# Optimization experiments

Hardware: AMD Instinct MI355X
Metric: run time of the kernel (lower is better)

The kernel has to match this reference:

```python
import jax, jax.numpy as jnp
import numpy as np

B, T, VOCAB = 65536, 34, 14
D_MODEL, TOK_DIM, POS_DIM, QK_DIM, FFN = 5, 2, 3, 5, 2
MAX_DIGITS = 10
EPS = 1e-5


def setup_inputs() -> dict:
    key = jax.random.key(0)
    ks = jax.random.split(key, 8)
    return dict(
        idx=jax.random.randint(ks[0], (B, T), 0, VOCAB),
        tok_A=jnp.float32(2.5), tok_start=jnp.float32(-1.2), tok_stride=jnp.float32(0.29),
        sp_amp=jnp.float32(3.5), sp_phase=jnp.float32(0.0), sp_slope=jnp.float32(0.15), sp_offset=jnp.float32(0.0),
        norm_w=jnp.ones((D_MODEL,), jnp.float32),
        q_w=jax.random.normal(ks[1], (QK_DIM, POS_DIM), jnp.float32) * 0.5,
        q_phase=jnp.zeros((1,), jnp.float32),
        out_A=jax.random.normal(ks[2], (D_MODEL, 1), jnp.float32) * 0.45,
        out_B=jax.random.normal(ks[3], (1, D_MODEL), jnp.float32) * 0.2,
        fc1_w=jax.random.normal(ks[4], (FFN, D_MODEL), jnp.float32) * 0.4,
        fc2_w=jax.random.normal(ks[5], (D_MODEL, FFN), jnp.float32) * 0.4,
        head_w=jax.random.normal(ks[6], (TOK_DIM, D_MODEL), jnp.float32) * 0.4,
    )


def rmsnorm(x, w):
    rms = jnp.sqrt(jnp.mean(x * x, axis=-1, keepdims=True) + EPS)
    return x / rms * w


def micro_forward(idx, tok_A, tok_start, tok_stride, sp_amp, sp_phase, sp_slope, sp_offset,
                  norm_w, q_w, q_phase, out_A, out_B, fc1_w, fc2_w, head_w):
    # token arc embedding table (V, 2)
    d = jnp.arange(VOCAB, dtype=jnp.float32)
    ang = tok_start + d * tok_stride
    tok_emb = jnp.stack([tok_A * jnp.cos(ang), tok_A * jnp.sin(ang)], axis=-1)
    # spiral positional embedding (T, 3)
    t = jnp.arange(T, dtype=jnp.float32)
    th = 2.0 * jnp.pi * t / MAX_DIGITS + sp_phase
    pos = jnp.stack([sp_amp * jnp.cos(th), sp_amp * jnp.sin(th), sp_slope * t + sp_offset], axis=-1)
    # embed: concat token (B,T,2) + position (T,3) -> (B,T,5)
    x = jnp.concatenate([tok_emb[idx], jnp.broadcast_to(pos, (idx.shape[0], T, POS_DIM))], axis=-1)
    # attention (pre-norm); q/k from positions only (qk_input='pos'), shared across batch
    h = rmsnorm(x, norm_w)
    k = pos @ q_w.T                       # (T, QK)
    c, s = jnp.cos(q_phase[0]), jnp.sin(q_phase[0])
    q = k.at[:, 0].set(c * k[:, 0] - s * k[:, 1]).at[:, 1].set(s * k[:, 0] + c * k[:, 1])
    scores = (q @ k.T) / jnp.sqrt(jnp.float32(QK_DIM))   # (T, T)
    causal = jnp.tril(jnp.ones((T, T), bool))
    attn = jax.nn.softmax(jnp.where(causal, scores, -1e9), axis=-1)
    attn_out = jnp.einsum('ts,bsd->btd', attn, h)         # v = normed x (head_dim = d_model)
    x = x + (attn_out @ out_A) @ out_B                    # rank-1 out_proj, residual
    # FFN (pre-norm, 2 hidden units)
    h2 = rmsnorm(x, norm_w)
    x = x + jax.nn.relu(h2 @ fc1_w.T) @ fc2_w.T
    # head: project to token plane, read out against arc embedding table
    hf = rmsnorm(x, norm_w)
    logits = (hf @ head_w.T) @ tok_emb.T                  # (B, T, V)
    return logits


def reference(idx, tok_A, tok_start, tok_stride, sp_amp, sp_phase, sp_slope, sp_offset,
              norm_w, q_w, q_phase, out_A, out_B, fc1_w, fc2_w, head_w):
    return micro_forward(idx, tok_A, tok_start, tok_stride, sp_amp, sp_phase, sp_slope, sp_offset,
                         norm_w, q_w, q_phase, out_A, out_B, fc1_w, fc2_w, head_w)
```

## Files before the change

kernel.cpp:

```cpp
#include <hip/hip_runtime.h>
#include <math.h>

#define T 34
#define V 14
#define NT 256
#define NBLK 2176
#define NWAVES 8704
#define LIM (65536 * 34)

typedef float f32x4 __attribute__((ext_vector_type(4)));


__global__ void setup_k(const float* __restrict__ tokA_p, const float* __restrict__ tokStart_p,
                        const float* __restrict__ tokStride_p, const float* __restrict__ spAmp_p,
                        const float* __restrict__ spPhase_p, const float* __restrict__ spSlope_p,
                        const float* __restrict__ spOffset_p, const float* __restrict__ norm_w,
                        const float* __restrict__ q_w, const float* __restrict__ q_phase,
                        const float* __restrict__ out_A, float* __restrict__ ws)
{
    __shared__ float sPOS[T][3];
    __shared__ float sK[T][5];
    __shared__ float sQ[T][5];
    __shared__ float sTE[V][2];
    __shared__ float sA[T][35];

    const int tid = threadIdx.x;

    if (tid < V) {
        float ang = tokStart_p[0] + (float)tid * tokStride_p[0];
        float c = tokA_p[0] * cosf(ang), s = tokA_p[0] * sinf(ang);
        sTE[tid][0] = c; sTE[tid][1] = s;
        ws[1680 + 2 * tid] = c; ws[1681 + 2 * tid] = s;
    }
    if (tid < T) {
        float th = (float)tid * 0.62831853071795864769f + spPhase_p[0];
        float p0 = spAmp_p[0] * cosf(th), p1 = spAmp_p[0] * sinf(th);
        float p2 = spSlope_p[0] * (float)tid + spOffset_p[0];
        sPOS[tid][0] = p0; sPOS[tid][1] = p1; sPOS[tid][2] = p2;
        ws[1708 + 3 * tid] = p0; ws[1709 + 3 * tid] = p1; ws[1710 + 3 * tid] = p2;
        float kk[5];
        #pragma unroll
        for (int i = 0; i < 5; ++i)
            kk[i] = p0 * q_w[3 * i] + p1 * q_w[3 * i + 1] + p2 * q_w[3 * i + 2];
        float cc = cosf(q_phase[0]), ss = sinf(q_phase[0]);
        #pragma unroll
        for (int i = 0; i < 5; ++i) sK[tid][i] = kk[i];
        sQ[tid][0] = cc * kk[0] - ss * kk[1];
        sQ[tid][1] = ss * kk[0] + cc * kk[1];
        sQ[tid][2] = kk[2]; sQ[tid][3] = kk[3]; sQ[tid][4] = kk[4];
    }
    __syncthreads();

    if (tid < T) {
        const int t = tid;
        float mx = -1e30f;
        for (int s = 0; s <= t; ++s) {
            float d = (sQ[t][0] * sK[s][0] + sQ[t][1] * sK[s][1] + sQ[t][2] * sK[s][2]
                     + sQ[t][3] * sK[s][3] + sQ[t][4] * sK[s][4]) * 0.44721359549995793928f;
            sA[t][s] = d;
            mx = fmaxf(mx, d);
        }
        float sum = 0.f;
        for (int s = 0; s <= t; ++s) { float e = expf(sA[t][s] - mx); sA[t][s] = e; sum += e; }
        float inv = 1.f / sum;
        for (int s = 0; s < 35; ++s) ws[t * 35 + s] = (s <= t) ? sA[t][s] * inv : 0.f;
    }
    for (int e = tid; e < 490; e += 64) {
        int v = e / 35, s = e - v * 35;
        float g = 0.f;
        if (s < T) {
            float x0 = sTE[v][0], x1 = sTE[v][1];
            float x2 = sPOS[s][0], x3 = sPOS[s][1], x4 = sPOS[s][2];
            float ms = (x0*x0 + x1*x1 + x2*x2 + x3*x3 + x4*x4) * 0.2f;
            float r = rsqrtf(ms + 1e-5f);
            g = (x0 * norm_w[0] * out_A[0] + x1 * norm_w[1] * out_A[1]
               + x2 * norm_w[2] * out_A[2] + x3 * norm_w[3] * out_A[3]
               + x4 * norm_w[4] * out_A[4]) * r;
        }
        ws[1190 + e] = g;
    }
}

__global__ __launch_bounds__(NT, 4) void micro_main(
    const int* __restrict__ idx, const float* __restrict__ ws, float* __restrict__ out,
    const float* __restrict__ norm_w, const float* __restrict__ out_B,
    const float* __restrict__ fc1_w, const float* __restrict__ fc2_w,
    const float* __restrict__ head_w)
{
    __shared__ float G_lds[V * 35];
    __shared__ float TE_lds[V * 2];
    __shared__ float gbW[4][2][104];
    __shared__ float stageAll[4 * 896];

    const int tid = threadIdx.x;
    const int w = tid >> 6, lane = tid & 63;
    const int wid = blockIdx.x * 4 + w;

    for (int i = tid; i < 490; i += NT) G_lds[i] = ws[1190 + i];
    if (tid < 28) TE_lds[tid] = ws[1680 + tid];
    __syncthreads();

    const int t = (wid * 64 + lane) % T;
    float A[T];
    #pragma unroll
    for (int s = 0; s < T; ++s) A[s] = ws[t * 35 + s];
    const float ps0 = ws[1708 + 3 * t], ps1 = ws[1709 + 3 * t], ps2 = ws[1710 + 3 * t];

    const float nw0 = norm_w[0], nw1 = norm_w[1], nw2 = norm_w[2], nw3 = norm_w[3], nw4 = norm_w[4];
    const float oB0 = out_B[0], oB1 = out_B[1], oB2 = out_B[2], oB3 = out_B[3], oB4 = out_B[4];
    float w1[2][5], hw[2][5], w20[5], w21[5];
    #pragma unroll
    for (int j = 0; j < 2; ++j)
        #pragma unroll
        for (int d = 0; d < 5; ++d) { w1[j][d] = fc1_w[j*5+d]; hw[j][d] = head_w[j*5+d]; }
    #pragma unroll
    for (int d = 0; d < 5; ++d) { w20[d] = fc2_w[2*d]; w21[d] = fc2_w[2*d+1]; }
    float te0[V], te1[V];
    #pragma unroll
    for (int v = 0; v < V; ++v) { te0[v] = ws[1680 + 2*v]; te1[v] = ws[1681 + 2*v]; }

    const int s_a = (lane < T) ? lane : lane - T;
    const int i2 = lane + 64;
    const int s_b = (i2 < 68) ? i2 - 34 : i2 - 68;
    const bool act2 = (i2 < 102);

    float* gbA = gbW[w][0];
    float* gbB = gbW[w][1];
    float* stg = stageAll + w * 896;
    float2* stg2 = reinterpret_cast<float2*>(stg);
    const f32x4* st4 = reinterpret_cast<const f32x4*>(stg);

    auto computeItem = [&](int tile, int rbase, int curtok, const float* gbT) {
        float acc0 = 0.f, acc1 = 0.f;
        const float2* gbp = reinterpret_cast<const float2*>(gbT + rbase);
        #pragma unroll
        for (int s = 0; s < 17; ++s) {
            float2 gg = gbp[s];
            acc0 = fmaf(A[2*s],   gg.x, acc0);
            acc1 = fmaf(A[2*s+1], gg.y, acc1);
        }
        float acc = acc0 + acc1;

        float2 te = *reinterpret_cast<const float2*>(&TE_lds[curtok * 2]);
        float x0 = te.x + acc * oB0;
        float x1 = te.y + acc * oB1;
        float x2 = ps0 + acc * oB2;
        float x3 = ps1 + acc * oB3;
        float x4 = ps2 + acc * oB4;

        float ms = (x0*x0 + x1*x1 + x2*x2 + x3*x3 + x4*x4) * 0.2f;
        float rr = rsqrtf(ms + 1e-5f);
        float h0 = x0*rr*nw0, h1 = x1*rr*nw1, h2 = x2*rr*nw2, h3 = x3*rr*nw3, h4 = x4*rr*nw4;
        float f0 = fmaxf(0.f, h0*w1[0][0] + h1*w1[0][1] + h2*w1[0][2] + h3*w1[0][3] + h4*w1[0][4]);
        float f1 = fmaxf(0.f, h0*w1[1][0] + h1*w1[1][1] + h2*w1[1][2] + h3*w1[1][3] + h4*w1[1][4]);
        x0 += f0*w20[0] + f1*w21[0];
        x1 += f0*w20[1] + f1*w21[1];
        x2 += f0*w20[2] + f1*w21[2];
        x3 += f0*w20[3] + f1*w21[3];
        x4 += f0*w20[4] + f1*w21[4];

        ms = (x0*x0 + x1*x1 + x2*x2 + x3*x3 + x4*x4) * 0.2f;
        rr = rsqrtf(ms + 1e-5f);
        h0 = x0*rr*nw0; h1 = x1*rr*nw1; h2 = x2*rr*nw2; h3 = x3*rr*nw3; h4 = x4*rr*nw4;
        float p0 = h0*hw[0][0] + h1*hw[0][1] + h2*hw[0][2] + h3*hw[0][3] + h4*hw[0][4];
        float p1 = h0*hw[1][0] + h1*hw[1][1] + h2*hw[1][2] + h3*hw[1][3] + h4*hw[1][4];

        #pragma unroll
        for (int j = 0; j < 7; ++j) {
            float2 o2;
            o2.x = p0 * te0[2*j]   + p1 * te1[2*j];
            o2.y = p0 * te0[2*j+1] + p1 * te1[2*j+1];
            stg2[lane * 7 + j] = o2;
        }
        f32x4* outp = reinterpret_cast<f32x4*>(out) + (size_t)tile * 224;
        __builtin_nontemporal_store(st4[lane],       outp + lane);
        __builtin_nontemporal_store(st4[lane + 64],  outp + lane + 64);
        __builtin_nontemporal_store(st4[lane + 128], outp + lane + 128);
        if (lane < 32)
            __builtin_nontemporal_store(st4[lane + 192], outp + lane + 192);
    };

    int tileA = wid, tileB = wid + NWAVES;
    int b0A = (tileA * 64) / T, b0B = (tileB * 64) / T;
    int tk0A = idx[b0A * T + lane];
    int tk1A = idx[min(b0A * T + lane + 64, LIM - 1)];
    int tkoA = idx[tileA * 64 + lane];
    int tk0B = idx[b0B * T + lane];
    int tk1B = idx[min(b0B * T + lane + 64, LIM - 1)];
    int tkoB = idx[tileB * 64 + lane];

    #pragma unroll
    for (int it = 0; it < 2; ++it) {
        gbA[lane] = G_lds[tk0A * 35 + s_a];
        if (act2) gbA[i2] = G_lds[tk1A * 35 + s_b];
        gbB[lane] = G_lds[tk0B * 35 + s_a];
        if (act2) gbB[i2] = G_lds[tk1B * 35 + s_b];

        const int rbA = ((tileA * 64 + lane) / T - b0A) * T;
        const int rbB = ((tileB * 64 + lane) / T - b0B) * T;
        const int ctA = tkoA, ctB = tkoB;
        const int tA = tileA, tB = tileB;

        if (it == 0) {
            tileA += 2 * NWAVES; tileB += 2 * NWAVES;
            b0A = (tileA * 64) / T; b0B = (tileB * 64) / T;
            tk0A = idx[b0A * T + lane];
            tk1A = idx[min(b0A * T + lane + 64, LIM - 1)];
            tkoA = idx[tileA * 64 + lane];
            tk0B = idx[b0B * T + lane];
            tk1B = idx[min(b0B * T + lane + 64, LIM - 1)];
            tkoB = idx[tileB * 64 + lane];
        }

        computeItem(tA, rbA, ctA, gbA);
        computeItem(tB, rbB, ctB, gbB);
    }
}

extern "C" void kernel_launch(void* const* d_in, const int* in_sizes, int n_in,
                              void* d_out, int out_size, void* d_ws, size_t ws_size,
                              hipStream_t stream) {
    const int*   idx        = (const int*)  d_in[0];
    const float* tok_A      = (const float*)d_in[1];
    const float* tok_start  = (const float*)d_in[2];
    const float* tok_stride = (const float*)d_in[3];
    const float* sp_amp     = (const float*)d_in[4];
    const float* sp_phase   = (const float*)d_in[5];
    const float* sp_slope   = (const float*)d_in[6];
    const float* sp_offset  = (const float*)d_in[7];
    const float* norm_w     = (const float*)d_in[8];
    const float* q_w        = (const float*)d_in[9];
    const float* q_phase    = (const float*)d_in[10];
    const float* out_A      = (const float*)d_in[11];
    const float* out_B      = (const float*)d_in[12];
    const float* fc1_w      = (const float*)d_in[13];
    const float* fc2_w      = (const float*)d_in[14];
    const float* head_w     = (const float*)d_in[15];
    float* out = (float*)d_out;
    float* ws  = (float*)d_ws;

    setup_k<<<1, 64, 0, stream>>>(tok_A, tok_start, tok_stride, sp_amp, sp_phase,
                                  sp_slope, sp_offset, norm_w, q_w, q_phase, out_A, ws);
    micro_main<<<NBLK, NT, 0, stream>>>(idx, ws, out, norm_w, out_B, fc1_w, fc2_w, head_w);
}
```

Baseline: 39.57 us.

## Fuse setup kernel into main kernel, recomputing shared tables per block

Removes the separate single-block setup launch and its workspace round trip. Each block of the main kernel now computes the token and position embeddings, the causal softmax attention matrix and the G table in LDS, and reuses the staging buffer as scratch for this. This drops one launch and the serial dependency on a tiny one-block kernel. In exchange every block repeats the setup arithmetic (trig, exp and the 34x34 scores) and adds extra barriers before the main work.

```diff
diff --git a/kernel.cpp b/kernel.cpp
--- a/kernel.cpp
+++ b/kernel.cpp
@@ -10,101 +10,111 @@
 
 typedef float f32x4 __attribute__((ext_vector_type(4)));
 
-
-__global__ void setup_k(const float* __restrict__ tokA_p, const float* __restrict__ tokStart_p,
-                        const float* __restrict__ tokStride_p, const float* __restrict__ spAmp_p,
-                        const float* __restrict__ spPhase_p, const float* __restrict__ spSlope_p,
-                        const float* __restrict__ spOffset_p, const float* __restrict__ norm_w,
-                        const float* __restrict__ q_w, const float* __restrict__ q_phase,
-                        const float* __restrict__ out_A, float* __restrict__ ws)
+__global__ __launch_bounds__(NT, 4) void micro_fused(
+    const int* __restrict__ idx, float* __restrict__ out,
+    const float* __restrict__ p_tokA, const float* __restrict__ p_tokStart,
+    const float* __restrict__ p_tokStride, const float* __restrict__ p_spAmp,
+    const float* __restrict__ p_spPhase, const float* __restrict__ p_spSlope,
+    const float* __restrict__ p_spOffset, const float* __restrict__ norm_w,
+    const float* __restrict__ q_w, const float* __restrict__ q_phase,
+    const float* __restrict__ out_A, const float* __restrict__ out_B,
+    const float* __restrict__ fc1_w, const float* __restrict__ fc2_w,
+    const float* __restrict__ head_w)
 {
-    __shared__ float sPOS[T][3];
-    __shared__ float sK[T][5];
-    __shared__ float sQ[T][5];
-    __shared__ float sTE[V][2];
-    __shared__ float sA[T][35];
+    __shared__ float G_lds[V * 35];
+    __shared__ float TE_lds[V * 2];
+    __shared__ float POS_lds[T * 3];
+    __shared__ float gbW[4][2][104];
+    __shared__ float stageAll[4 * 896];
 
     const int tid = threadIdx.x;
+    const int w = tid >> 6, lane = tid & 63;
+    const int wid = blockIdx.x * 4 + w;
+
+    float* sA = stageAll;
+    float* sK = stageAll + 1200;
+    float* sQ = stageAll + 1370;
 
     if (tid < V) {
-        float ang = tokStart_p[0] + (float)tid * tokStride_p[0];
-        float c = tokA_p[0] * cosf(ang), s = tokA_p[0] * sinf(ang);
-        sTE[tid][0] = c; sTE[tid][1] = s;
-        ws[1680 + 2 * tid] = c; ws[1681 + 2 * tid] = s;
+        float ang = p_tokStart[0] + (float)tid * p_tokStride[0];
+        TE_lds[2 * tid]     = p_tokA[0] * cosf(ang);
+        TE_lds[2 * tid + 1] = p_tokA[0] * sinf(ang);
     }
     if (tid < T) {
-        float th = (float)tid * 0.62831853071795864769f + spPhase_p[0];
-        float p0 = spAmp_p[0] * cosf(th), p1 = spAmp_p[0] * sinf(th);
-        float p2 = spSlope_p[0] * (float)tid + spOffset_p[0];
-        sPOS[tid][0] = p0; sPOS[tid][1] = p1; sPOS[tid][2] = p2;
-        ws[1708 + 3 * tid] = p0; ws[1709 + 3 * tid] = p1; ws[1710 + 3 * tid] = p2;
+        float th = (float)tid * 0.62831853071795864769f + p_spPhase[0];
+        float p0 = p_spAmp[0] * cosf(th), p1 = p_spAmp[0] * sinf(th);
+        float p2 = p_spSlope[0] * (float)tid + p_spOffset[0];
+        POS_lds[3 * tid] = p0; POS_lds[3 * tid + 1] = p1; POS_lds[3 * tid + 2] = p2;
         float kk[5];
         #pragma unroll
         for (int i = 0; i < 5; ++i)
             kk[i] = p0 * q_w[3 * i] + p1 * q_w[3 * i + 1] + p2 * q_w[3 * i + 2];
         float cc = cosf(q_phase[0]), ss = sinf(q_phase[0]);
         #pragma unroll
-        for (int i = 0; i < 5; ++i) sK[tid][i] = kk[i];
-        sQ[tid][0] = cc * kk[0] - ss * kk[1];
-        sQ[tid][1] = ss * kk[0] + cc * kk[1];
-        sQ[tid][2] = kk[2]; sQ[tid][3] = kk[3]; sQ[tid][4] = kk[4];
-    }
-    __syncthreads();
-
-    if (tid < T) {
-        const int t = tid;
-        float mx = -1e30f;
-        for (int s = 0; s <= t; ++s) {
-            float d = (sQ[t][0] * sK[s][0] + sQ[t][1] * sK[s][1] + sQ[t][2] * sK[s][2]
-                     + sQ[t][3] * sK[s][3] + sQ[t][4] * sK[s][4]) * 0.44721359549995793928f;
-            sA[t][s] = d;
-            mx = fmaxf(mx, d);
-        }
-        float sum = 0.f;
-        for (int s = 0; s <= t; ++s) { float e = expf(sA[t][s] - mx); sA[t][s] = e; sum += e; }
-        float inv = 1.f / sum;
-        for (int s = 0; s < 35; ++s) ws[t * 35 + s] = (s <= t) ? sA[t][s] * inv : 0.f;
-    }
-    for (int e = tid; e < 490; e += 64) {
+        for (int i = 0; i < 5; ++i) sK[tid * 5 + i] = kk[i];
+        sQ[tid * 5 + 0] = cc * kk[0] - ss * kk[1];
+        sQ[tid * 5 + 1] = ss * kk[0] + cc * kk[1];
+        sQ[tid * 5 + 2] = kk[2]; sQ[tid * 5 + 3] = kk[3]; sQ[tid * 5 + 4] = kk[4];
+    }
+    __syncthreads();
+
+    for (int e = tid; e < T * T; e += NT) {
+        unsigned tt = (unsigned)e / (unsigned)T;
+        unsigned s  = (unsigned)e - tt * T;
+        if (s <= tt) {
+            float d = 0.f;
+            #pragma unroll
+            for (int i = 0; i < 5; ++i) d += sQ[tt * 5 + i] * sK[s * 5 + i];
+            sA[tt * 35 + s] = d * 0.44721359549995793928f;
+        }
+    }
+    for (int e = tid; e < V * 35; e += NT) {
         int v = e / 35, s = e - v * 35;
         float g = 0.f;
         if (s < T) {
-            float x0 = sTE[v][0], x1 = sTE[v][1];
-            float x2 = sPOS[s][0], x3 = sPOS[s][1], x4 = sPOS[s][2];
+            float x0 = TE_lds[2*v], x1 = TE_lds[2*v+1];
+            float x2 = POS_lds[3*s], x3 = POS_lds[3*s+1], x4 = POS_lds[3*s+2];
             float ms = (x0*x0 + x1*x1 + x2*x2 + x3*x3 + x4*x4) * 0.2f;
             float r = rsqrtf(ms + 1e-5f);
             g = (x0 * norm_w[0] * out_A[0] + x1 * norm_w[1] * out_A[1]
                + x2 * norm_w[2] * out_A[2] + x3 * norm_w[3] * out_A[3]
                + x4 * norm_w[4] * out_A[4]) * r;
         }
-        ws[1190 + e] = g;
-    }
-}
-
-__global__ __launch_bounds__(NT, 4) void micro_main(
-    const int* __restrict__ idx, const float* __restrict__ ws, float* __restrict__ out,
-    const float* __restrict__ norm_w, const float* __restrict__ out_B,
-    const float* __restrict__ fc1_w, const float* __restrict__ fc2_w,
-    const float* __restrict__ head_w)
-{
-    __shared__ float G_lds[V * 35];
-    __shared__ float TE_lds[V * 2];
-    __shared__ float gbW[4][2][104];
-    __shared__ float stageAll[4 * 896];
-
-    const int tid = threadIdx.x;
-    const int w = tid >> 6, lane = tid & 63;
-    const int wid = blockIdx.x * 4 + w;
-
-    for (int i = tid; i < 490; i += NT) G_lds[i] = ws[1190 + i];
-    if (tid < 28) TE_lds[tid] = ws[1680 + tid];
+        G_lds[e] = g;
+    }
+    __syncthreads();
+
+    if (tid < T) {
+        const int tt = tid;
+        float vals[T];
+        #pragma unroll
+        for (int s = 0; s < T; ++s) vals[s] = sA[tt * 35 + s];
+        float mx = -1e30f;
+        #pragma unroll
+        for (int s = 0; s < T; ++s) if (s <= tt) mx = fmaxf(mx, vals[s]);
+        float sum = 0.f;
+        #pragma unroll
+        for (int s = 0; s < T; ++s) {
+            float e2 = (s <= tt) ? expf(vals[s] - mx) : 0.f;
+            vals[s] = e2;
+            sum += e2;
+        }
+        float inv = 1.f / sum;
+        #pragma unroll
+        for (int s = 0; s < T; ++s) sA[tt * 35 + s] = vals[s] * inv;
+        sA[tt * 35 + 34] = 0.f;
+    }
     __syncthreads();
 
     const int t = (wid * 64 + lane) % T;
     float A[T];
     #pragma unroll
-    for (int s = 0; s < T; ++s) A[s] = ws[t * 35 + s];
-    const float ps0 = ws[1708 + 3 * t], ps1 = ws[1709 + 3 * t], ps2 = ws[1710 + 3 * t];
+    for (int s = 0; s < T; ++s) A[s] = sA[t * 35 + s];
+    const float ps0 = POS_lds[3*t], ps1 = POS_lds[3*t+1], ps2 = POS_lds[3*t+2];
+    float te0[V], te1[V];
+    #pragma unroll
+    for (int v = 0; v < V; ++v) { te0[v] = TE_lds[2*v]; te1[v] = TE_lds[2*v+1]; }
+    __syncthreads();
 
     const float nw0 = norm_w[0], nw1 = norm_w[1], nw2 = norm_w[2], nw3 = norm_w[3], nw4 = norm_w[4];
     const float oB0 = out_B[0], oB1 = out_B[1], oB2 = out_B[2], oB3 = out_B[3], oB4 = out_B[4];
@@ -115,9 +125,6 @@
         for (int d = 0; d < 5; ++d) { w1[j][d] = fc1_w[j*5+d]; hw[j][d] = head_w[j*5+d]; }
     #pragma unroll
     for (int d = 0; d < 5; ++d) { w20[d] = fc2_w[2*d]; w21[d] = fc2_w[2*d+1]; }
-    float te0[V], te1[V];
-    #pragma unroll
-    for (int v = 0; v < V; ++v) { te0[v] = ws[1680 + 2*v]; te1[v] = ws[1681 + 2*v]; }
 
     const int s_a = (lane < T) ? lane : lane - T;
     const int i2 = lane + 64;
@@ -237,9 +244,9 @@
     const float* fc2_w      = (const float*)d_in[14];
     const float* head_w     = (const float*)d_in[15];
     float* out = (float*)d_out;
-    float* ws  = (float*)d_ws;
-
-    setup_k<<<1, 64, 0, stream>>>(tok_A, tok_start, tok_stride, sp_amp, sp_phase,
-                                  sp_slope, sp_offset, norm_w, q_w, q_phase, out_A, ws);
-    micro_main<<<NBLK, NT, 0, stream>>>(idx, ws, out, norm_w, out_B, fc1_w, fc2_w, head_w);
+
+    micro_fused<<<NBLK, NT, 0, stream>>>(idx, out, tok_A, tok_start, tok_stride,
+                                         sp_amp, sp_phase, sp_slope, sp_offset,
+                                         norm_w, q_w, q_phase, out_A, out_B,
+                                         fc1_w, fc2_w, head_w);
 }
```

Measured after the change: 37.43 us. 1.06x faster.
